# Kernel optimization log

Hardware: AMD Instinct MI355X
Metric: run time of the kernel (lower is better)

The kernel has to match this reference:

```python
import jax, jax.numpy as jnp
import numpy as np

N, E = 100000, 1600000
D_IN, D_E, D_OUT, D_HID = 64, 64, 64, 128


def setup_inputs() -> dict:
    key = jax.random.key(0)
    ks = jax.random.split(key, 12)
    s = 0.05
    return {
        "nfeats": jax.random.normal(ks[0], (N, 1, D_IN), jnp.float32),
        "efeats": jax.random.normal(ks[1], (E, 1, D_E), jnp.float32),
        "src": jax.random.randint(ks[2], (E,), 0, N, jnp.int32),
        "dst": jax.random.randint(ks[3], (E,), 0, N, jnp.int32),
        "W1_msg": jax.random.normal(ks[4], (D_IN + D_E, D_HID), jnp.float32) * s,
        "b1_msg": jnp.zeros((D_HID,), jnp.float32),
        "W1_apply": jax.random.normal(ks[5], (D_IN + D_HID, D_HID), jnp.float32) * s,
        "b1_apply": jnp.zeros((D_HID,), jnp.float32),
        "W2_msg": jax.random.normal(ks[6], (D_HID + D_E, D_OUT), jnp.float32) * s,
        "b2_msg": jnp.zeros((D_OUT,), jnp.float32),
        "W2_apply": jax.random.normal(ks[7], (D_HID + D_OUT, D_OUT), jnp.float32) * s,
        "b2_apply": jnp.zeros((D_OUT,), jnp.float32),
    }


def _gcn_layer(x, e, src, dst, n_nodes, inv_deg, Wm, bm, Wa, ba):
    # gather src node feats, concat edge feats, linear message: [E, d_out]
    m = jnp.concatenate([x[src], e], axis=-1) @ Wm + bm
    # mean-aggregate over destination nodes (0 for isolated nodes, like DGL)
    h_neigh = jax.ops.segment_sum(m, dst, num_segments=n_nodes) * inv_deg
    return jax.nn.relu(jnp.concatenate([x, h_neigh], axis=-1) @ Wa + ba)


def reference(nfeats, efeats, src, dst, W1_msg, b1_msg, W1_apply, b1_apply,
              W2_msg, b2_msg, W2_apply, b2_apply):
    n_nodes = nfeats.shape[0]
    x = nfeats[:, 0, :]  # squeeze singleton dim (final .sum(1) removes it anyway)
    e = efeats[:, 0, :]
    deg = jax.ops.segment_sum(jnp.ones_like(dst, dtype=x.dtype), dst,
                              num_segments=n_nodes)
    inv_deg = (jnp.where(deg > 0, 1.0 / jnp.maximum(deg, 1.0), 0.0))[:, None]
    x = _gcn_layer(x, e, src, dst, n_nodes, inv_deg, W1_msg, b1_msg, W1_apply, b1_apply)
    # dropout is identity in eval mode
    x = _gcn_layer(x, e, src, dst, n_nodes, inv_deg, W2_msg, b2_msg, W2_apply, b2_apply)
    return x  # [N, ndim_out] == nfeats.sum(1) since middle dim is 1
```

## Files before the change

kernel.cpp:

```cpp
#include <hip/hip_runtime.h>
#include <hip/hip_bf16.h>

#define NN 100000
#define EE 1600000
#define CAP 96

typedef __attribute__((ext_vector_type(8))) short bf16x8;
typedef __attribute__((ext_vector_type(4))) float f32x4;
typedef __attribute__((ext_vector_type(4))) unsigned int u32x4;
typedef __attribute__((ext_vector_type(2))) unsigned int u32x2;

__device__ __forceinline__ unsigned int f2bf(float x) {
    union { float f; unsigned int u; } v; v.f = x;
    return (v.u + 0x7fffu + ((v.u >> 16) & 1u)) >> 16;
}
__device__ __forceinline__ unsigned int pack2(float a, float b) {
    return f2bf(a) | (f2bf(b) << 16);
}
__device__ __forceinline__ float bf2f(unsigned short s) {
    unsigned int u = ((unsigned int)s) << 16;
    return __builtin_bit_cast(float, u);
}

__device__ __forceinline__ void packW_body(const float* __restrict__ W,
                                           u32x4* __restrict__ pW,
                                           int KC, int NT, int NOUT, int g) {
    if (g >= NT * KC * 64) return;
    int lane = g & 63;
    int rest = g >> 6;
    int kc = rest % KC;
    int nt = rest / KC;
    int k0 = kc * 32 + ((lane >> 4) << 3);
    int n  = nt * 16 + (lane & 15);
    u32x4 u;
    #pragma unroll
    for (int t = 0; t < 4; ++t)
        u[t] = pack2(W[(k0 + 2 * t) * NOUT + n], W[(k0 + 2 * t + 1) * NOUT + n]);
    pW[g] = u;
}

__global__ void k_init(int* __restrict__ cnt,
                       const float* __restrict__ W1m, u32x4* __restrict__ pW1m,
                       const float* __restrict__ W1a, u32x4* __restrict__ pW1a,
                       const float* __restrict__ W2m, u32x4* __restrict__ pW2m,
                       const float* __restrict__ W2a, u32x4* __restrict__ pW2a) {
    const int b = blockIdx.x;
    const int t = threadIdx.x;
    if (b < 391) {
        int i = b * 256 + t;
        if (i < NN) cnt[i] = 0;
    } else if (b < 399) {
        packW_body(W1m, pW1m, 4, 8, 128, (b - 391) * 256 + t);
    } else if (b < 411) {
        packW_body(W1a, pW1a, 6, 8, 128, (b - 399) * 256 + t);
    } else if (b < 417) {
        packW_body(W2m, pW2m, 6, 4, 64, (b - 411) * 256 + t);
    } else {
        packW_body(W2a, pW2a, 6, 4, 64, (b - 417) * 256 + t);
    }
}

__global__ void k_bucket(const int* __restrict__ dst, const int* __restrict__ src,
                         int* __restrict__ cnt, int2* __restrict__ ep2) {
    int e = blockIdx.x * 256 + threadIdx.x;
    if (e < EE) {
        const int d = dst[e];
        const int p = atomicAdd(&cnt[d], 1);
        if (p < CAP) ep2[(size_t)d * CAP + p] = make_int2(e, src[e]);
    }
}

__global__ __launch_bounds__(256)
void k_agg01(const float* __restrict__ efeats, const float* __restrict__ nfeats,
             const int2* __restrict__ ep2, const int* __restrict__ cnt,
             unsigned short* __restrict__ eaggm, unsigned short* __restrict__ xaggm1)
{
    const int v = blockIdx.x * 4 + (threadIdx.x >> 6);
    if (v >= NN) return;
    const int lane = threadIdx.x & 63;
    const int s_ = lane >> 4;
    const int c  = lane & 15;
    const int dc = cnt[v];
    const int d  = (dc < CAP) ? dc : CAP;
    const int2* bp = ep2 + (size_t)v * CAP;

    float ae[4], ax[4];
    #pragma unroll
    for (int q = 0; q < 4; ++q) { ae[q] = 0.f; ax[q] = 0.f; }

    for (int it = s_; it < d; it += 16) {
        const int j1 = it + 4, j2 = it + 8, j3 = it + 12;
        const bool h1 = (j1 < d), h2 = (j2 < d), h3 = (j3 < d);
        const int2 p0 = bp[it];
        const int2 p1 = h1 ? bp[j1] : p0;
        const int2 p2 = h2 ? bp[j2] : p0;
        const int2 p3 = h3 ? bp[j3] : p0;
        f32x4 ue0 = *(const f32x4*)(efeats + (size_t)p0.x * 64 + c * 4);
        f32x4 ux0 = *(const f32x4*)(nfeats + (size_t)p0.y * 64 + c * 4);
        f32x4 ue1 = *(const f32x4*)(efeats + (size_t)p1.x * 64 + c * 4);
        f32x4 ux1 = *(const f32x4*)(nfeats + (size_t)p1.y * 64 + c * 4);
        f32x4 ue2 = *(const f32x4*)(efeats + (size_t)p2.x * 64 + c * 4);
        f32x4 ux2 = *(const f32x4*)(nfeats + (size_t)p2.y * 64 + c * 4);
        f32x4 ue3 = *(const f32x4*)(efeats + (size_t)p3.x * 64 + c * 4);
        f32x4 ux3 = *(const f32x4*)(nfeats + (size_t)p3.y * 64 + c * 4);
        const float m1 = h1 ? 1.f : 0.f;
        const float m2 = h2 ? 1.f : 0.f;
        const float m3 = h3 ? 1.f : 0.f;
        #pragma unroll
        for (int q = 0; q < 4; ++q) {
            ae[q] += ue0[q] + m1 * ue1[q] + m2 * ue2[q] + m3 * ue3[q];
            ax[q] += ux0[q] + m1 * ux1[q] + m2 * ux2[q] + m3 * ux3[q];
        }
    }
    #pragma unroll
    for (int q = 0; q < 4; ++q) {
        ae[q] += __shfl_xor(ae[q], 16);
        ae[q] += __shfl_xor(ae[q], 32);
        ax[q] += __shfl_xor(ax[q], 16);
        ax[q] += __shfl_xor(ax[q], 32);
    }
    if (s_ == 0) {
        const float iv = (dc > 0) ? (1.0f / (float)dc) : 0.f;
        u32x2 oe, ox;
        oe[0] = pack2(ae[0] * iv, ae[1] * iv);
        oe[1] = pack2(ae[2] * iv, ae[3] * iv);
        ox[0] = pack2(ax[0] * iv, ax[1] * iv);
        ox[1] = pack2(ax[2] * iv, ax[3] * iv);
        *(u32x2*)(eaggm  + (size_t)v * 64 + c * 4) = oe;
        *(u32x2*)(xaggm1 + (size_t)v * 64 + c * 4) = ox;
    }
}

__global__ __launch_bounds__(256)
void k_agg2y(const unsigned short* __restrict__ y, const int2* __restrict__ ep2,
             const int* __restrict__ cnt, unsigned short* __restrict__ xagg2y)
{
    const int v = blockIdx.x * 4 + (threadIdx.x >> 6);
    if (v >= NN) return;
    const int lane = threadIdx.x & 63;
    const int s_ = lane >> 3;
    const int c  = lane & 7;
    const int dc = cnt[v];
    const int d  = (dc < CAP) ? dc : CAP;
    const int2* bp = ep2 + (size_t)v * CAP;

    float acc[8];
    #pragma unroll
    for (int q = 0; q < 8; ++q) acc[q] = 0.f;

    for (int it = s_; it < d; it += 16) {
        const int j1 = it + 8;
        const int2 p0 = bp[it];
        const bool h1 = (j1 < d);
        const int2 p1 = h1 ? bp[j1] : p0;
        bf16x8 u0 = *(const bf16x8*)(y + (size_t)p0.y * 64 + c * 8);
        bf16x8 u1 = *(const bf16x8*)(y + (size_t)p1.y * 64 + c * 8);
        const float m1 = h1 ? 1.f : 0.f;
        #pragma unroll
        for (int q = 0; q < 8; ++q)
            acc[q] += bf2f((unsigned short)u0[q]) + m1 * bf2f((unsigned short)u1[q]);
    }
    #pragma unroll
    for (int q = 0; q < 8; ++q) {
        acc[q] += __shfl_xor(acc[q], 8);
        acc[q] += __shfl_xor(acc[q], 16);
        acc[q] += __shfl_xor(acc[q], 32);
    }
    if (s_ == 0) {
        const float iv = (dc > 0) ? (1.0f / (float)dc) : 0.f;
        u32x4 o;
        #pragma unroll
        for (int t = 0; t < 4; ++t) o[t] = pack2(acc[2*t] * iv, acc[2*t+1] * iv);
        *(u32x4*)(xagg2y + (size_t)v * 64 + c * 8) = o;
    }
}

__global__ __launch_bounds__(256)
void k_gl1(const float* __restrict__ nfeats,
           const unsigned short* __restrict__ xaggm1, const unsigned short* __restrict__ eaggm,
           const int* __restrict__ cnt,
           const float* __restrict__ b1m, const float* __restrict__ b1a,
           const float* __restrict__ b2m,
           const u32x4* __restrict__ pW1m, const u32x4* __restrict__ pW1a,
           const u32x4* __restrict__ pW2m,
           unsigned short* __restrict__ x1, unsigned short* __restrict__ y,
           unsigned short* __restrict__ ew2)
{
    __shared__ __align__(16) u32x4 A4[128 * 24];
    unsigned short* AS = (unsigned short*)A4;

    const int tid  = threadIdx.x;
    const int lane = tid & 63;
    const int w    = tid >> 6;
    const int tileM = blockIdx.x * 128;

    for (int idx = tid; idx < 128 * 16; idx += 256) {
        const int row = idx >> 4;
        const int u   = idx & 15;
        const int gr  = tileM + row;
        u32x4 o; o[0]=o[1]=o[2]=o[3]=0u;
        if (gr < NN) {
            o = (u < 8) ? *(const u32x4*)(xaggm1 + (size_t)gr * 64 + u * 8)
                        : *(const u32x4*)(eaggm  + (size_t)gr * 64 + (u - 8) * 8);
        }
        A4[row * 16 + (u ^ (row & 7))] = o;
    }
    __syncthreads();

    const int rowBase = (w >> 1) * 64;
    const int ctBase  = (w & 1) * 4;
    const int ctBase2 = (w & 1) * 2;
    const int lrow    = lane & 15;
    const int kq      = lane >> 4;

    f32x4 acc[4][4];
    f32x4 acc3[4][2];
    #pragma unroll
    for (int mt = 0; mt < 4; ++mt) {
        #pragma unroll
        for (int nt = 0; nt < 4; ++nt)
            #pragma unroll
            for (int q = 0; q < 4; ++q) acc[mt][nt][q] = 0.f;
        #pragma unroll
        for (int nt = 0; nt < 2; ++nt)
            #pragma unroll
            for (int q = 0; q < 4; ++q) acc3[mt][nt][q] = 0.f;
    }

    #pragma unroll
    for (int kc = 0; kc < 4; ++kc) {
        bf16x8 a[4];
        #pragma unroll
        for (int mt = 0; mt < 4; ++mt) {
            const int row = rowBase + mt * 16 + lrow;
            a[mt] = __builtin_bit_cast(bf16x8, A4[row * 16 + ((kc * 4 + kq) ^ (row & 7))]);
        }
        #pragma unroll
        for (int nt = 0; nt < 4; ++nt) {
            bf16x8 b = __builtin_bit_cast(bf16x8, pW1m[(size_t)((ctBase + nt) * 4 + kc) * 64 + lane]);
            #pragma unroll
            for (int mt = 0; mt < 4; ++mt)
                acc[mt][nt] = __builtin_amdgcn_mfma_f32_16x16x32_bf16(a[mt], b, acc[mt][nt], 0, 0, 0);
        }
        if (kc >= 2) {
            #pragma unroll
            for (int nt = 0; nt < 2; ++nt) {
                bf16x8 b = __builtin_bit_cast(bf16x8, pW2m[(size_t)((ctBase2 + nt) * 6 + kc + 2) * 64 + lane]);
                #pragma unroll
                for (int mt = 0; mt < 4; ++mt)
                    acc3[mt][nt] = __builtin_amdgcn_mfma_f32_16x16x32_bf16(a[mt], b, acc3[mt][nt], 0, 0, 0);
            }
        }
    }
    __syncthreads();

    for (int idx = tid; idx < 128 * 8; idx += 256) {
        const int row = idx >> 3;
        const int u   = idx & 7;
        const int gr  = tileM + row;
        u32x4 o; o[0]=o[1]=o[2]=o[3]=0u;
        if (gr < NN) {
            const f32x4* pv = (const f32x4*)(nfeats + (size_t)gr * 64 + u * 8);
            f32x4 f0 = pv[0], f1 = pv[1];
            o[0] = pack2(f0[0], f0[1]); o[1] = pack2(f0[2], f0[3]);
            o[2] = pack2(f1[0], f1[1]); o[3] = pack2(f1[2], f1[3]);
        }
        A4[row * 24 + (u ^ (row & 7))] = o;
    }
    {
        float bb[4], bb2[2];
        #pragma unroll
        for (int nt = 0; nt < 4; ++nt) bb[nt] = b1m[(ctBase + nt) * 16 + lrow];
        #pragma unroll
        for (int nt = 0; nt < 2; ++nt) bb2[nt] = b2m[(ctBase2 + nt) * 16 + lrow];
        #pragma unroll
        for (int mt = 0; mt < 4; ++mt) {
            #pragma unroll
            for (int j = 0; j < 4; ++j) {
                const int r  = rowBase + mt * 16 + kq * 4 + j;
                const int gr = tileM + r;
                const float msk = (gr < NN && cnt[gr] > 0) ? 1.f : 0.f;
                #pragma unroll
                for (int nt = 0; nt < 4; ++nt) {
                    const int col = 64 + (ctBase + nt) * 16 + lrow;
                    const float val = acc[mt][nt][j] + bb[nt] * msk;
                    AS[(r * 24 + ((col >> 3) ^ (r & 7))) * 8 + (col & 7)] = (unsigned short)f2bf(val);
                }
                if (gr < NN) {
                    #pragma unroll
                    for (int nt = 0; nt < 2; ++nt) {
                        const int col2 = (ctBase2 + nt) * 16 + lrow;
                        ew2[(size_t)gr * 64 + col2] =
                            (unsigned short)f2bf(acc3[mt][nt][j] + bb2[nt] * msk);
                    }
                }
            }
        }
    }
    __syncthreads();

    f32x4 acc2[4][4];
    #pragma unroll
    for (int mt = 0; mt < 4; ++mt)
        #pragma unroll
        for (int nt = 0; nt < 4; ++nt)
            #pragma unroll
            for (int q = 0; q < 4; ++q) acc2[mt][nt][q] = 0.f;

    #pragma unroll
    for (int kc = 0; kc < 6; ++kc) {
        bf16x8 a[4];
        #pragma unroll
        for (int mt = 0; mt < 4; ++mt) {
            const int row = rowBase + mt * 16 + lrow;
            a[mt] = __builtin_bit_cast(bf16x8, A4[row * 24 + ((kc * 4 + kq) ^ (row & 7))]);
        }
        #pragma unroll
        for (int nt = 0; nt < 4; ++nt) {
            bf16x8 b = __builtin_bit_cast(bf16x8, pW1a[(size_t)((ctBase + nt) * 6 + kc) * 64 + lane]);
            #pragma unroll
            for (int mt = 0; mt < 4; ++mt)
                acc2[mt][nt] = __builtin_amdgcn_mfma_f32_16x16x32_bf16(a[mt], b, acc2[mt][nt], 0, 0, 0);
        }
    }

    {
        float bb[4];
        #pragma unroll
        for (int nt = 0; nt < 4; ++nt) bb[nt] = b1a[(ctBase + nt) * 16 + lrow];
        #pragma unroll
        for (int mt = 0; mt < 4; ++mt) {
            #pragma unroll
            for (int j = 0; j < 4; ++j) {
                const int gr = tileM + rowBase + mt * 16 + kq * 4 + j;
                if (gr < NN) {
                    #pragma unroll
                    for (int nt = 0; nt < 4; ++nt) {
                        const float v = fmaxf(acc2[mt][nt][j] + bb[nt], 0.f);
                        x1[(size_t)gr * 128 + (ctBase + nt) * 16 + lrow] = (unsigned short)f2bf(v);
                    }
                }
            }
        }
    }
    __syncthreads();

    {
        float bb[4];
        #pragma unroll
        for (int nt = 0; nt < 4; ++nt) bb[nt] = b1a[(ctBase + nt) * 16 + lrow];
        #pragma unroll
        for (int mt = 0; mt < 4; ++mt) {
            #pragma unroll
            for (int j = 0; j < 4; ++j) {
                const int r = rowBase + mt * 16 + kq * 4 + j;
                #pragma unroll
                for (int nt = 0; nt < 4; ++nt) {
                    const int col = (ctBase + nt) * 16 + lrow;
                    const float v = fmaxf(acc2[mt][nt][j] + bb[nt], 0.f);
                    AS[(r * 16 + ((col >> 3) ^ (r & 7))) * 8 + (col & 7)] = (unsigned short)f2bf(v);
                }
            }
        }
    }
    __syncthreads();

    f32x4 acc4[4][2];
    #pragma unroll
    for (int mt = 0; mt < 4; ++mt)
        #pragma unroll
        for (int nt = 0; nt < 2; ++nt)
            #pragma unroll
            for (int q = 0; q < 4; ++q) acc4[mt][nt][q] = 0.f;

    #pragma unroll
    for (int kc = 0; kc < 4; ++kc) {
        bf16x8 a[4];
        #pragma unroll
        for (int mt = 0; mt < 4; ++mt) {
            const int row = rowBase + mt * 16 + lrow;
            a[mt] = __builtin_bit_cast(bf16x8, A4[row * 16 + ((kc * 4 + kq) ^ (row & 7))]);
        }
        #pragma unroll
        for (int nt = 0; nt < 2; ++nt) {
            bf16x8 b = __builtin_bit_cast(bf16x8, pW2m[(size_t)((ctBase2 + nt) * 6 + kc) * 64 + lane]);
            #pragma unroll
            for (int mt = 0; mt < 4; ++mt)
                acc4[mt][nt] = __builtin_amdgcn_mfma_f32_16x16x32_bf16(a[mt], b, acc4[mt][nt], 0, 0, 0);
        }
    }
    #pragma unroll
    for (int mt = 0; mt < 4; ++mt) {
        #pragma unroll
        for (int j = 0; j < 4; ++j) {
            const int gr = tileM + rowBase + mt * 16 + kq * 4 + j;
            if (gr < NN) {
                #pragma unroll
                for (int nt = 0; nt < 2; ++nt)
                    y[(size_t)gr * 64 + (ctBase2 + nt) * 16 + lrow] =
                        (unsigned short)f2bf(acc4[mt][nt][j]);
            }
        }
    }
}

__global__ __launch_bounds__(256)
void k_gl2(const unsigned short* __restrict__ x1,
           const unsigned short* __restrict__ xagg2y, const unsigned short* __restrict__ ew2,
           const float* __restrict__ b2a, const u32x4* __restrict__ pW2a,
           float* __restrict__ out)
{
    __shared__ __align__(16) u32x4 A4[128 * 24];

    const int tid  = threadIdx.x;
    const int lane = tid & 63;
    const int w    = tid >> 6;
    const int tileM = blockIdx.x * 128;

    for (int idx = tid; idx < 128 * 16; idx += 256) {
        const int row = idx >> 4;
        const int u   = idx & 15;
        const int gr  = tileM + row;
        u32x4 o; o[0]=o[1]=o[2]=o[3]=0u;
        if (gr < NN) o = *(const u32x4*)(x1 + (size_t)gr * 128 + u * 8);
        A4[row * 24 + (u ^ (row & 7))] = o;
    }
    for (int idx = tid; idx < 128 * 8; idx += 256) {
        const int row = idx >> 3;
        const int u   = idx & 7;
        const int gr  = tileM + row;
        u32x4 o; o[0]=o[1]=o[2]=o[3]=0u;
        if (gr < NN) {
            u32x4 ua = *(const u32x4*)(xagg2y + (size_t)gr * 64 + u * 8);
            u32x4 ub = *(const u32x4*)(ew2    + (size_t)gr * 64 + u * 8);
            #pragma unroll
            for (int t = 0; t < 4; ++t) {
                const float lo = bf2f((unsigned short)(ua[t] & 0xffffu))
                               + bf2f((unsigned short)(ub[t] & 0xffffu));
                const float hi = bf2f((unsigned short)(ua[t] >> 16))
                               + bf2f((unsigned short)(ub[t] >> 16));
                o[t] = pack2(lo, hi);
            }
        }
        A4[row * 24 + ((16 + u) ^ (row & 7))] = o;
    }
    __syncthreads();

    const int rowBase = (w >> 1) * 64;
    const int ctBase  = (w & 1) * 2;
    const int lrow    = lane & 15;
    const int kq      = lane >> 4;

    f32x4 acc[4][2];
    #pragma unroll
    for (int mt = 0; mt < 4; ++mt)
        #pragma unroll
        for (int nt = 0; nt < 2; ++nt)
            #pragma unroll
            for (int q = 0; q < 4; ++q) acc[mt][nt][q] = 0.f;

    #pragma unroll
    for (int kc = 0; kc < 6; ++kc) {
        bf16x8 a[4];
        #pragma unroll
        for (int mt = 0; mt < 4; ++mt) {
            const int row = rowBase + mt * 16 + lrow;
            a[mt] = __builtin_bit_cast(bf16x8, A4[row * 24 + ((kc * 4 + kq) ^ (row & 7))]);
        }
        #pragma unroll
        for (int nt = 0; nt < 2; ++nt) {
            bf16x8 b = __builtin_bit_cast(bf16x8, pW2a[(size_t)((ctBase + nt) * 6 + kc) * 64 + lane]);
            #pragma unroll
            for (int mt = 0; mt < 4; ++mt)
                acc[mt][nt] = __builtin_amdgcn_mfma_f32_16x16x32_bf16(a[mt], b, acc[mt][nt], 0, 0, 0);
        }
    }
    {
        float bb[2];
        #pragma unroll
        for (int nt = 0; nt < 2; ++nt) bb[nt] = b2a[(ctBase + nt) * 16 + lrow];
        #pragma unroll
        for (int mt = 0; mt < 4; ++mt) {
            #pragma unroll
            for (int j = 0; j < 4; ++j) {
                const int gr = tileM + rowBase + mt * 16 + kq * 4 + j;
                if (gr < NN) {
                    #pragma unroll
                    for (int nt = 0; nt < 2; ++nt) {
                        const float v = fmaxf(acc[mt][nt][j] + bb[nt], 0.f);
                        out[(size_t)gr * 64 + (ctBase + nt) * 16 + lrow] = v;
                    }
                }
            }
        }
    }
}

extern "C" void kernel_launch(void* const* d_in, const int* in_sizes, int n_in,
                              void* d_out, int out_size, void* d_ws, size_t ws_size,
                              hipStream_t stream) {
    const float* nfeats = (const float*)d_in[0];
    const float* efeats = (const float*)d_in[1];
    const int*   src    = (const int*)d_in[2];
    const int*   dst    = (const int*)d_in[3];
    const float* W1m = (const float*)d_in[4];
    const float* b1m = (const float*)d_in[5];
    const float* W1a = (const float*)d_in[6];
    const float* b1a = (const float*)d_in[7];
    const float* W2m = (const float*)d_in[8];
    const float* b2m = (const float*)d_in[9];
    const float* W2a = (const float*)d_in[10];
    const float* b2a = (const float*)d_in[11];
    float* out = (float*)d_out;

    char* ws = (char*)d_ws;
    unsigned short* eaggm  = (unsigned short*)(ws + 0);
    unsigned short* xaggm1 = (unsigned short*)(ws + 12800000);
    unsigned short* y      = (unsigned short*)(ws + 25600000);
    unsigned short* ew2    = (unsigned short*)(ws + 38400000);
    unsigned short* xagg2y = (unsigned short*)(ws + 51200000);
    unsigned short* x1     = (unsigned short*)(ws + 64000000);
    int2*           ep2    = (int2*)(ws + 89600000);
    int*            cnt    = (int*)(ws + 166400000);
    u32x4* pW1m = (u32x4*)(ws + 166800000);
    u32x4* pW1a = (u32x4*)(ws + 166832768);
    u32x4* pW2m = (u32x4*)(ws + 166881920);
    u32x4* pW2a = (u32x4*)(ws + 166906496);

    k_init<<<423, 256, 0, stream>>>(cnt, W1m, pW1m, W1a, pW1a, W2m, pW2m, W2a, pW2a);
    k_bucket<<<(EE + 255) / 256, 256, 0, stream>>>(dst, src, cnt, ep2);

    const int NBAGG = NN / 4;
    const int NBG   = (NN + 127) / 128;

    k_agg01<<<NBAGG, 256, 0, stream>>>(efeats, nfeats, ep2, cnt, eaggm, xaggm1);
    k_gl1<<<NBG, 256, 0, stream>>>(nfeats, xaggm1, eaggm, cnt, b1m, b1a, b2m,
                                   pW1m, pW1a, pW2m, x1, y, ew2);
    k_agg2y<<<NBAGG, 256, 0, stream>>>(y, ep2, cnt, xagg2y);
    k_gl2<<<NBG, 256, 0, stream>>>(x1, xagg2y, ew2, b2a, pW2a, out);
}
```

Baseline: 358.9 us.

## Compute layer-2 self term in gl1 and drop x1 round-trip; shrink bucket CAP

The layer-2 apply product x1·W2a[0:128] now runs inside k_gl1 while x1 is still in shared memory, and is written as a 64-wide bf16 partial o1. This replaces the 128-wide x1 store and reload, so k_gl2 only multiplies the 64-wide aggregated input and adds o1. The bucket capacity CAP drops from 96 to 64, shrinking the edge-pair buffer and its footprint. The cost is an extra bf16 rounding of the partial sum, plus a risk of overflow if any node's in-degree exceeds 64.

```diff
diff --git a/kernel.cpp b/kernel.cpp
--- a/kernel.cpp
+++ b/kernel.cpp
@@ -3,7 +3,7 @@
 
 #define NN 100000
 #define EE 1600000
-#define CAP 96
+#define CAP 64
 
 typedef __attribute__((ext_vector_type(8))) short bf16x8;
 typedef __attribute__((ext_vector_type(4))) float f32x4;
@@ -182,8 +182,8 @@
            const float* __restrict__ b1m, const float* __restrict__ b1a,
            const float* __restrict__ b2m,
            const u32x4* __restrict__ pW1m, const u32x4* __restrict__ pW1a,
-           const u32x4* __restrict__ pW2m,
-           unsigned short* __restrict__ x1, unsigned short* __restrict__ y,
+           const u32x4* __restrict__ pW2m, const u32x4* __restrict__ pW2a,
+           unsigned short* __restrict__ y, unsigned short* __restrict__ o1,
            unsigned short* __restrict__ ew2)
 {
     __shared__ __align__(16) u32x4 A4[128 * 24];
@@ -323,26 +323,6 @@
                 acc2[mt][nt] = __builtin_amdgcn_mfma_f32_16x16x32_bf16(a[mt], b, acc2[mt][nt], 0, 0, 0);
         }
     }
-
-    {
-        float bb[4];
-        #pragma unroll
-        for (int nt = 0; nt < 4; ++nt) bb[nt] = b1a[(ctBase + nt) * 16 + lrow];
-        #pragma unroll
-        for (int mt = 0; mt < 4; ++mt) {
-            #pragma unroll
-            for (int j = 0; j < 4; ++j) {
-                const int gr = tileM + rowBase + mt * 16 + kq * 4 + j;
-                if (gr < NN) {
-                    #pragma unroll
-                    for (int nt = 0; nt < 4; ++nt) {
-                        const float v = fmaxf(acc2[mt][nt][j] + bb[nt], 0.f);
-                        x1[(size_t)gr * 128 + (ctBase + nt) * 16 + lrow] = (unsigned short)f2bf(v);
-                    }
-                }
-            }
-        }
-    }
     __syncthreads();
 
     {
@@ -365,13 +345,13 @@
     }
     __syncthreads();
 
-    f32x4 acc4[4][2];
+    f32x4 acc4[4][2], acc5[4][2];
     #pragma unroll
     for (int mt = 0; mt < 4; ++mt)
         #pragma unroll
         for (int nt = 0; nt < 2; ++nt)
             #pragma unroll
-            for (int q = 0; q < 4; ++q) acc4[mt][nt][q] = 0.f;
+            for (int q = 0; q < 4; ++q) { acc4[mt][nt][q] = 0.f; acc5[mt][nt][q] = 0.f; }
 
     #pragma unroll
     for (int kc = 0; kc < 4; ++kc) {
@@ -383,10 +363,13 @@
         }
         #pragma unroll
         for (int nt = 0; nt < 2; ++nt) {
-            bf16x8 b = __builtin_bit_cast(bf16x8, pW2m[(size_t)((ctBase2 + nt) * 6 + kc) * 64 + lane]);
-            #pragma unroll
-            for (int mt = 0; mt < 4; ++mt)
-                acc4[mt][nt] = __builtin_amdgcn_mfma_f32_16x16x32_bf16(a[mt], b, acc4[mt][nt], 0, 0, 0);
+            bf16x8 bm = __builtin_bit_cast(bf16x8, pW2m[(size_t)((ctBase2 + nt) * 6 + kc) * 64 + lane]);
+            bf16x8 ba = __builtin_bit_cast(bf16x8, pW2a[(size_t)((ctBase2 + nt) * 6 + kc) * 64 + lane]);
+            #pragma unroll
+            for (int mt = 0; mt < 4; ++mt) {
+                acc4[mt][nt] = __builtin_amdgcn_mfma_f32_16x16x32_bf16(a[mt], bm, acc4[mt][nt], 0, 0, 0);
+                acc5[mt][nt] = __builtin_amdgcn_mfma_f32_16x16x32_bf16(a[mt], ba, acc5[mt][nt], 0, 0, 0);
+            }
         }
     }
     #pragma unroll
@@ -396,35 +379,29 @@
             const int gr = tileM + rowBase + mt * 16 + kq * 4 + j;
             if (gr < NN) {
                 #pragma unroll
-                for (int nt = 0; nt < 2; ++nt)
-                    y[(size_t)gr * 64 + (ctBase2 + nt) * 16 + lrow] =
-                        (unsigned short)f2bf(acc4[mt][nt][j]);
+                for (int nt = 0; nt < 2; ++nt) {
+                    const int col = (ctBase2 + nt) * 16 + lrow;
+                    y [(size_t)gr * 64 + col] = (unsigned short)f2bf(acc4[mt][nt][j]);
+                    o1[(size_t)gr * 64 + col] = (unsigned short)f2bf(acc5[mt][nt][j]);
+                }
             }
         }
     }
 }
 
 __global__ __launch_bounds__(256)
-void k_gl2(const unsigned short* __restrict__ x1,
+void k_gl2(const unsigned short* __restrict__ o1,
            const unsigned short* __restrict__ xagg2y, const unsigned short* __restrict__ ew2,
            const float* __restrict__ b2a, const u32x4* __restrict__ pW2a,
            float* __restrict__ out)
 {
-    __shared__ __align__(16) u32x4 A4[128 * 24];
+    __shared__ __align__(16) u32x4 A4[128 * 8];
 
     const int tid  = threadIdx.x;
     const int lane = tid & 63;
     const int w    = tid >> 6;
     const int tileM = blockIdx.x * 128;
 
-    for (int idx = tid; idx < 128 * 16; idx += 256) {
-        const int row = idx >> 4;
-        const int u   = idx & 15;
-        const int gr  = tileM + row;
-        u32x4 o; o[0]=o[1]=o[2]=o[3]=0u;
-        if (gr < NN) o = *(const u32x4*)(x1 + (size_t)gr * 128 + u * 8);
-        A4[row * 24 + (u ^ (row & 7))] = o;
-    }
     for (int idx = tid; idx < 128 * 8; idx += 256) {
         const int row = idx >> 3;
         const int u   = idx & 7;
@@ -442,7 +419,7 @@
                 o[t] = pack2(lo, hi);
             }
         }
-        A4[row * 24 + ((16 + u) ^ (row & 7))] = o;
+        A4[row * 8 + (u ^ (row & 7))] = o;
     }
     __syncthreads();
 
@@ -460,16 +437,16 @@
             for (int q = 0; q < 4; ++q) acc[mt][nt][q] = 0.f;
 
     #pragma unroll
-    for (int kc = 0; kc < 6; ++kc) {
+    for (int kc = 0; kc < 2; ++kc) {
         bf16x8 a[4];
         #pragma unroll
         for (int mt = 0; mt < 4; ++mt) {
             const int row = rowBase + mt * 16 + lrow;
-            a[mt] = __builtin_bit_cast(bf16x8, A4[row * 24 + ((kc * 4 + kq) ^ (row & 7))]);
+            a[mt] = __builtin_bit_cast(bf16x8, A4[row * 8 + ((kc * 4 + kq) ^ (row & 7))]);
         }
         #pragma unroll
         for (int nt = 0; nt < 2; ++nt) {
-            bf16x8 b = __builtin_bit_cast(bf16x8, pW2a[(size_t)((ctBase + nt) * 6 + kc) * 64 + lane]);
+            bf16x8 b = __builtin_bit_cast(bf16x8, pW2a[(size_t)((ctBase + nt) * 6 + 4 + kc) * 64 + lane]);
             #pragma unroll
             for (int mt = 0; mt < 4; ++mt)
                 acc[mt][nt] = __builtin_amdgcn_mfma_f32_16x16x32_bf16(a[mt], b, acc[mt][nt], 0, 0, 0);
@@ -487,8 +464,9 @@
                 if (gr < NN) {
                     #pragma unroll
                     for (int nt = 0; nt < 2; ++nt) {
-                        const float v = fmaxf(acc[mt][nt][j] + bb[nt], 0.f);
-                        out[(size_t)gr * 64 + (ctBase + nt) * 16 + lrow] = v;
+                        const int col = (ctBase + nt) * 16 + lrow;
+                        const float v = fmaxf(acc[mt][nt][j] + bf2f(o1[(size_t)gr * 64 + col]) + bb[nt], 0.f);
+                        out[(size_t)gr * 64 + col] = v;
                     }
                 }
             }
@@ -519,13 +497,13 @@
     unsigned short* y      = (unsigned short*)(ws + 25600000);
     unsigned short* ew2    = (unsigned short*)(ws + 38400000);
     unsigned short* xagg2y = (unsigned short*)(ws + 51200000);
-    unsigned short* x1     = (unsigned short*)(ws + 64000000);
-    int2*           ep2    = (int2*)(ws + 89600000);
-    int*            cnt    = (int*)(ws + 166400000);
-    u32x4* pW1m = (u32x4*)(ws + 166800000);
-    u32x4* pW1a = (u32x4*)(ws + 166832768);
-    u32x4* pW2m = (u32x4*)(ws + 166881920);
-    u32x4* pW2a = (u32x4*)(ws + 166906496);
+    unsigned short* o1     = (unsigned short*)(ws + 64000000);
+    int2*           ep2    = (int2*)(ws + 76800000);
+    int*            cnt    = (int*)(ws + 128000000);
+    u32x4* pW1m = (u32x4*)(ws + 128400000);
+    u32x4* pW1a = (u32x4*)(ws + 128432768);
+    u32x4* pW2m = (u32x4*)(ws + 128481920);
+    u32x4* pW2a = (u32x4*)(ws + 128506496);
 
     k_init<<<423, 256, 0, stream>>>(cnt, W1m, pW1m, W1a, pW1a, W2m, pW2m, W2a, pW2a);
     k_bucket<<<(EE + 255) / 256, 256, 0, stream>>>(dst, src, cnt, ep2);
@@ -535,7 +513,7 @@
 
     k_agg01<<<NBAGG, 256, 0, stream>>>(efeats, nfeats, ep2, cnt, eaggm, xaggm1);
     k_gl1<<<NBG, 256, 0, stream>>>(nfeats, xaggm1, eaggm, cnt, b1m, b1a, b2m,
-                                   pW1m, pW1a, pW2m, x1, y, ew2);
+                                   pW1m, pW1a, pW2m, pW2a, y, o1, ew2);
     k_agg2y<<<NBAGG, 256, 0, stream>>>(y, ep2, cnt, xagg2y);
-    k_gl2<<<NBG, 256, 0, stream>>>(x1, xagg2y, ew2, b2a, pW2a, out);
-}
+    k_gl2<<<NBG, 256, 0, stream>>>(o1, xagg2y, ew2, b2a, pW2a, out);
+}
```

After: 356.2 us. About the same (-0.7%).
